# Performance work log

Measured on AMD Instinct MI355X. Metric: run time of the kernel, lower is better.

## Reference

```python
import jax, jax.numpy as jnp
import numpy as np

B, L, C = 8, 1024, 1024
H, DK = 16, 64
E, HID = 16, 64
CAP_FACTOR = 0.5
EPS = 1e-5


def setup_inputs() -> dict:
    key = jax.random.key(0)
    ks = jax.random.split(key, 20)
    f32 = jnp.float32
    s_c = 1.0 / np.sqrt(C)
    s_h = 1.0 / np.sqrt(HID)
    inp = {
        "qx": jax.random.normal(ks[0], (B, L, C), f32),
        "kx": jax.random.normal(ks[1], (B, L, C), f32),
        "vx": jax.random.normal(ks[2], (B, L, C), f32),
        "maskPAD": jnp.ones((B, L), dtype=bool),
        # attention params (torch Linear weight layout [out,in])
        "WQ": jax.random.normal(ks[3], (H * DK, C), f32) * s_c,
        "bQ": jnp.zeros((H * DK,), f32),
        "WK": jax.random.normal(ks[4], (H * DK, C), f32) * s_c,
        "bK": jnp.zeros((H * DK,), f32),
        "WV": jax.random.normal(ks[5], (H * DK, C), f32) * s_c,
        "bV": jnp.zeros((H * DK,), f32),
        "WO": jax.random.normal(ks[6], (C, H * DK), f32) * s_c,
        "bO": jnp.zeros((C,), f32),
        "ln1_w": jnp.ones((C,), f32),
        "ln1_b": jnp.zeros((C,), f32),
        # router
        "Wsw": jax.random.normal(ks[7], (E, C), f32) * s_c,
        "bsw": jnp.zeros((E,), f32),
        # per-expert FFN: Linear(C,HID) -> ReLU -> Linear(HID,C)
        "W1": jax.random.normal(ks[8], (E, C, HID), f32) * s_c,
        "b1": jnp.zeros((E, HID), f32),
        "W2": jax.random.normal(ks[9], (E, HID, C), f32) * s_h,
        "b2": jnp.zeros((E, C), f32),
    }
    return inp


def _layernorm(x, w, b):
    mu = jnp.mean(x, axis=-1, keepdims=True)
    var = jnp.mean(jnp.square(x - mu), axis=-1, keepdims=True)
    return (x - mu) * jax.lax.rsqrt(var + EPS) * w + b


def _moe(x2d, Wsw, bsw, W1, b1, W2, b2):
    # x2d: [N, C] tokens; top-1 switch routing with capacity-based token dropping
    N = x2d.shape[0]
    cap = int(CAP_FACTOR * N / E)
    logits = x2d @ Wsw.T + bsw                      # [N, E]
    probs = jax.nn.softmax(logits, axis=-1)
    routes = jnp.argmax(probs, axis=-1)             # [N]
    pmax = jnp.max(probs, axis=-1)                  # [N]
    onehot = jax.nn.one_hot(routes, E, dtype=jnp.int32)
    # position of each token within its expert's queue (deterministic order;
    # torch uses randperm before dropping -- math identical up to permutation)
    pos = jnp.take_along_axis(jnp.cumsum(onehot, axis=0) - 1, routes[:, None], axis=1)[:, 0]
    kept = pos < cap
    slot = jnp.where(kept, routes * cap + pos, E * cap)  # dropped -> trash slot
    buf = jnp.zeros((E * cap + 1, x2d.shape[1]), x2d.dtype).at[slot].set(x2d)
    eb = buf[: E * cap].reshape(E, cap, -1)         # [E, cap, C]
    h = jax.nn.relu(jnp.einsum("ecd,edh->ech", eb, W1) + b1[:, None, :])
    y = jnp.einsum("ech,ehd->ecd", h, W2) + b2[:, None, :]
    yflat = y.reshape(E * cap, -1)
    gathered = yflat[jnp.where(kept, routes * cap + pos, 0)]
    final = jnp.where(kept[:, None], gathered, x2d)  # dropped tokens pass through
    # is_scale_prob=False: multiply by p/stop_grad(p) (==1 in fwd, grads flow)
    scale = pmax / jax.lax.stop_gradient(pmax)
    return final * scale[:, None]


def reference(qx, kx, vx, maskPAD, WQ, bQ, WK, bK, WV, bV, WO, bO,
              ln1_w, ln1_b, Wsw, bsw, W1, b1, W2, b2):
    # multi-head attention (maskPAD is unused in the original SelfAttention_1)
    q = (qx @ WQ.T + bQ).reshape(B, L, H, DK)
    k = (kx @ WK.T + bK).reshape(B, L, H, DK)
    v = (vx @ WV.T + bV).reshape(B, L, H, DK)
    scores = jnp.einsum("bqhd,bkhd->bhqk", q, k) / np.sqrt(DK).astype(np.float32)
    alpha = jax.nn.softmax(scores, axis=-1)
    z = jnp.einsum("bhqk,bkhd->bqhd", alpha, v).reshape(B, L, H * DK)
    att = z @ WO.T + bO
    zn = _layernorm(qx + att, ln1_w, ln1_b)          # norm1 residual
    moe_out = _moe(zn.reshape(B * L, C), Wsw, bsw, W1, b1, W2, b2).reshape(B, L, C)
    out = zn + moe_out                               # note: norm2 unused in original
    return (out, kx, vx, maskPAD)
```

## Files before the change

### kernel.cpp

```cpp
#include <hip/hip_runtime.h>


typedef __bf16 bf16;
typedef __bf16 bf16x4 __attribute__((ext_vector_type(4)));
typedef __bf16 bf16x8 __attribute__((ext_vector_type(8)));
typedef float  f32x4  __attribute__((ext_vector_type(4)));

#define NB    8
#define LL    1024
#define CC    1024
#define NH    16
#define DKD   64
#define NE    16
#define NHID  64
#define CAP   256
#define NTOK  (NB*LL)
#define MB    (1024*1024)

__device__ __forceinline__ void gload16(const bf16* g, bf16* l)
{
    __builtin_amdgcn_global_load_lds(
        (const __attribute__((address_space(1))) void*)g,
        (__attribute__((address_space(3))) void*)l, 16, 0, 0);
}

__device__ inline void split3v(const f32x4 v, bf16x4& a, bf16x4& b, bf16x4& c)
{
#pragma unroll
    for (int k = 0; k < 4; k++) {
        const float x  = v[k];
        const bf16  hi = (bf16)x;
        const float r1 = x - (float)hi;
        const bf16  md = (bf16)r1;
        const float r2 = r1 - (float)md;
        a[k] = hi; b[k] = md; c[k] = (bf16)r2;
    }
}

__device__ inline bf16x8 pack8(const bf16x4 a, const bf16x4 b)
{
    bf16x8 r;
#pragma unroll
    for (int e = 0; e < 4; e++) { r[e] = a[e]; r[4 + e] = b[e]; }
    return r;
}

__global__ __launch_bounds__(256)
void split3(const float* __restrict__ z, bf16* __restrict__ z1,
            bf16* __restrict__ z2, bf16* __restrict__ z3)
{
    const size_t i = ((size_t)blockIdx.x * 256 + threadIdx.x) * 4;
    const f32x4 v = *(const f32x4*)(z + i);
    bf16x4 a, b, c;
    split3v(v, a, b, c);
    *(bf16x4*)(z1 + i) = a;
    *(bf16x4*)(z2 + i) = b;
    *(bf16x4*)(z3 + i) = c;
}

__global__ __launch_bounds__(512)
void gemm_limb6(const bf16* __restrict__ A0, const bf16* __restrict__ A1,
                const bf16* __restrict__ A2,
                const bf16* __restrict__ W0, const bf16* __restrict__ W1l,
                const bf16* __restrict__ W2l,
                const float* __restrict__ bias, float* __restrict__ C,
                int M, int N, int K)
{
    __shared__ __align__(16) bf16 As[2][3][128][32];
    __shared__ __align__(16) bf16 Ws[2][3][128][32];

    const int tid  = threadIdx.x;
    const int lane = tid & 63;
    const int wv   = tid >> 6;
    const int bm = blockIdx.x * 128;
    const int bn = blockIdx.y * 128;
    const int wm = (wv & 1) * 64;
    const int wn = (wv >> 1) * 32;
    const int lr = lane & 15;
    const int lq = lane >> 4;

    const int r0  = tid >> 2;
    const int cc8 = (tid & 3) * 8;

    const bf16* Aps[3] = {A0, A1, A2};
    const bf16* Wps[3] = {W0, W1l, W2l};

    f32x4 acc[4][2];
#pragma unroll
    for (int i = 0; i < 4; i++)
#pragma unroll
        for (int j = 0; j < 2; j++) acc[i][j] = f32x4{0.f, 0.f, 0.f, 0.f};

    constexpr int PI[6] = {0, 0, 1, 1, 0, 2};
    constexpr int PJ[6] = {0, 1, 0, 1, 2, 0};

#pragma unroll
    for (int l = 0; l < 3; l++) {
        gload16(Aps[l] + (size_t)(bm + r0) * K + cc8, &As[0][l][r0][cc8]);
        gload16(Wps[l] + (size_t)(bn + r0) * K + cc8, &Ws[0][l][r0][cc8]);
    }
    __syncthreads();

    int cur = 0;
    const int NT = K / 32;
    for (int t = 0; t < NT; t++) {
        if (t < NT - 1) {
            const int k1 = (t + 1) * 32;
#pragma unroll
            for (int l = 0; l < 3; l++) {
                gload16(Aps[l] + (size_t)(bm + r0) * K + k1 + cc8,
                        &As[cur ^ 1][l][r0][cc8]);
                gload16(Wps[l] + (size_t)(bn + r0) * K + k1 + cc8,
                        &Ws[cur ^ 1][l][r0][cc8]);
            }
        }

        bf16x8 af[3][4], bfr[3][2];
#pragma unroll
        for (int i = 0; i < 4; i++) {
            af[0][i] = *(const bf16x8*)&As[cur][0][wm + i * 16 + lr][lq * 8];
            af[1][i] = *(const bf16x8*)&As[cur][1][wm + i * 16 + lr][lq * 8];
            af[2][i] = *(const bf16x8*)&As[cur][2][wm + i * 16 + lr][lq * 8];
        }
#pragma unroll
        for (int j = 0; j < 2; j++) {
            bfr[0][j] = *(const bf16x8*)&Ws[cur][0][wn + j * 16 + lr][lq * 8];
            bfr[1][j] = *(const bf16x8*)&Ws[cur][1][wn + j * 16 + lr][lq * 8];
            bfr[2][j] = *(const bf16x8*)&Ws[cur][2][wn + j * 16 + lr][lq * 8];
        }
#pragma unroll
        for (int p = 0; p < 6; p++)
#pragma unroll
            for (int i = 0; i < 4; i++)
#pragma unroll
                for (int j = 0; j < 2; j++)
                    acc[i][j] = __builtin_amdgcn_mfma_f32_16x16x32_bf16(
                        af[PI[p]][i], bfr[PJ[p]][j], acc[i][j], 0, 0, 0);

        __syncthreads();
        cur ^= 1;
    }

#pragma unroll
    for (int i = 0; i < 4; i++)
#pragma unroll
        for (int j = 0; j < 2; j++) {
            const int col = bn + wn + j * 16 + lr;
            const float bv = bias[col];
#pragma unroll
            for (int r = 0; r < 4; r++) {
                const int row = bm + wm + i * 16 + lq * 4 + r;
                C[(size_t)row * N + col] = acc[i][j][r] + bv;
            }
        }
}

__global__ __launch_bounds__(256)
void vsplit(const float* __restrict__ Vf, bf16* __restrict__ T0,
            bf16* __restrict__ T1, bf16* __restrict__ T2)
{
    __shared__ __align__(16) bf16 Lt[3][64][72];
    const int tid = threadIdx.x;
    const int bh  = blockIdx.x;
    const int b   = bh >> 4, h = bh & 15;
    const int l0  = blockIdx.y * 64;

    const int dql = tid & 15;
    const int lrr = tid >> 4;
#pragma unroll
    for (int p = 0; p < 4; p++) {
        const int l = p * 16 + lrr;
        const f32x4 v = *(const f32x4*)(
            Vf + (size_t)(b * LL + l0 + l) * 1024 + h * 64 + dql * 4);
        bf16x4 a, bq, c; split3v(v, a, bq, c);
#pragma unroll
        for (int e = 0; e < 4; e++) {
            Lt[0][dql * 4 + e][l] = a[e];
            Lt[1][dql * 4 + e][l] = bq[e];
            Lt[2][dql * 4 + e][l] = c[e];
        }
    }
    __syncthreads();
    const int d  = tid >> 2;
    const int lc = tid & 3;
    const size_t o = (size_t)bh * 65536 + (size_t)d * 1024 + l0 + lc * 16;
    *(bf16x8*)(T0 + o)     = *(const bf16x8*)&Lt[0][d][lc * 16];
    *(bf16x8*)(T0 + o + 8) = *(const bf16x8*)&Lt[0][d][lc * 16 + 8];
    *(bf16x8*)(T1 + o)     = *(const bf16x8*)&Lt[1][d][lc * 16];
    *(bf16x8*)(T1 + o + 8) = *(const bf16x8*)&Lt[1][d][lc * 16 + 8];
    *(bf16x8*)(T2 + o)     = *(const bf16x8*)&Lt[2][d][lc * 16];
    *(bf16x8*)(T2 + o + 8) = *(const bf16x8*)&Lt[2][d][lc * 16 + 8];
}

__global__ __launch_bounds__(256)
void flash_mfma(float* __restrict__ Qf, const float* __restrict__ Kf,
                const bf16* __restrict__ Vt0, const bf16* __restrict__ Vt1,
                const bf16* __restrict__ Vt2)
{
    __shared__ __align__(16) bf16  Ks[3][32][64];
    __shared__ __align__(16) bf16  Vs[3][64][32];
    __shared__ __align__(16) float Ps[128][32];

    const int tid  = threadIdx.x;
    const int lane = tid & 63;
    const int w    = tid >> 6;
    const int lr   = lane & 15;
    const int lq   = lane >> 4;
    const int lr7  = lr & 7;

    const int bid = (int)blockIdx.x;
    const int qb  = (bid >> 3) & 7;
    const int bh  = (bid & 7) * 16 + (bid >> 6);
    const int b   = bh >> 4, h = bh & 15;
    const int q0  = qb * 128;
    const size_t base = (size_t)b * LL * 1024 + (size_t)h * 64;

    bf16x8 qf[3][2][2];
#pragma unroll
    for (int mi = 0; mi < 2; mi++)
#pragma unroll
        for (int ks = 0; ks < 2; ks++) {
            const float* src = Qf + base +
                (size_t)(q0 + w * 32 + mi * 16 + lr) * 1024 + ks * 32 + lq * 8;
            f32x4 v0 = *(const f32x4*)src;
            f32x4 v1 = *(const f32x4*)(src + 4);
            v0 *= 0.125f; v1 *= 0.125f;
            bf16x4 a0, b0, c0, a1, b1, c1;
            split3v(v0, a0, b0, c0);
            split3v(v1, a1, b1, c1);
            qf[0][mi][ks] = pack8(a0, a1);
            qf[1][mi][ks] = pack8(b0, b1);
            qf[2][mi][ks] = pack8(c0, c1);
        }

    const int kr  = tid >> 3, kq = tid & 7;
    const int kpg = kq ^ (kr & 7);
    const int vr  = tid >> 2, vg = tid & 3;
    const int vlg = vg ^ ((vr >> 1) & 3);
    const float* kbase = Kf + base + (size_t)kr * 1024 + kq * 8;
    const size_t vtb = (size_t)bh * 65536 + (size_t)vr * 1024 + (size_t)vlg * 8;

    f32x4  kp0 = *(const f32x4*)(kbase);
    f32x4  kp1 = *(const f32x4*)(kbase + 4);
    bf16x8 vp0 = *(const bf16x8*)(Vt0 + vtb);
    bf16x8 vp1 = *(const bf16x8*)(Vt1 + vtb);
    bf16x8 vp2 = *(const bf16x8*)(Vt2 + vtb);

    float m_[2][4], l_[2][4];
    f32x4 accO[2][4];
#pragma unroll
    for (int mi = 0; mi < 2; mi++)
#pragma unroll
        for (int rr = 0; rr < 4; rr++) { m_[mi][rr] = -3.0e38f; l_[mi][rr] = 0.f; }
#pragma unroll
    for (int mi = 0; mi < 2; mi++)
#pragma unroll
        for (int nd = 0; nd < 4; nd++) accO[mi][nd] = f32x4{0.f, 0.f, 0.f, 0.f};

    constexpr int PI[6] = {0, 0, 1, 1, 0, 2};
    constexpr int PJ[6] = {0, 1, 0, 1, 2, 0};

    for (int kt = 0; kt < 32; kt++) {
        __syncthreads();
        {
            bf16x4 a0, b0, c0, a1, b1, c1;
            split3v(kp0, a0, b0, c0);
            split3v(kp1, a1, b1, c1);
            *(bf16x8*)&Ks[0][kr][kpg * 8] = pack8(a0, a1);
            *(bf16x8*)&Ks[1][kr][kpg * 8] = pack8(b0, b1);
            *(bf16x8*)&Ks[2][kr][kpg * 8] = pack8(c0, c1);
            *(bf16x8*)&Vs[0][vr][vg * 8] = vp0;
            *(bf16x8*)&Vs[1][vr][vg * 8] = vp1;
            *(bf16x8*)&Vs[2][vr][vg * 8] = vp2;
        }
        __syncthreads();
        if (kt < 31) {
            const float* ks_ = kbase + (size_t)(kt + 1) * 32 * 1024;
            kp0 = *(const f32x4*)ks_;
            kp1 = *(const f32x4*)(ks_ + 4);
            const size_t vo = vtb + (size_t)(kt + 1) * 32;
            vp0 = *(const bf16x8*)(Vt0 + vo);
            vp1 = *(const bf16x8*)(Vt1 + vo);
            vp2 = *(const bf16x8*)(Vt2 + vo);
        }

        f32x4 accS[2][2];
#pragma unroll
        for (int mi = 0; mi < 2; mi++)
#pragma unroll
            for (int nj = 0; nj < 2; nj++) accS[mi][nj] = f32x4{0.f, 0.f, 0.f, 0.f};
#pragma unroll
        for (int nj = 0; nj < 2; nj++) {
            bf16x8 kfr[3][2];
#pragma unroll
            for (int ks = 0; ks < 2; ks++) {
                const int kg = (ks * 4 + lq) ^ lr7;
                kfr[0][ks] = *(const bf16x8*)&Ks[0][nj * 16 + lr][kg * 8];
                kfr[1][ks] = *(const bf16x8*)&Ks[1][nj * 16 + lr][kg * 8];
                kfr[2][ks] = *(const bf16x8*)&Ks[2][nj * 16 + lr][kg * 8];
            }
#pragma unroll
            for (int p = 0; p < 6; p++)
#pragma unroll
                for (int mi = 0; mi < 2; mi++)
#pragma unroll
                    for (int ks = 0; ks < 2; ks++)
                        accS[mi][nj] = __builtin_amdgcn_mfma_f32_16x16x32_bf16(
                            qf[PI[p]][mi][ks], kfr[PJ[p]][ks], accS[mi][nj], 0, 0, 0);
        }

#pragma unroll
        for (int mi = 0; mi < 2; mi++)
#pragma unroll
            for (int rr = 0; rr < 4; rr++) {
                const float s0 = accS[mi][0][rr], s1 = accS[mi][1][rr];
                float t = fmaxf(s0, s1);
                t = fmaxf(t, __shfl_xor(t, 1));
                t = fmaxf(t, __shfl_xor(t, 2));
                t = fmaxf(t, __shfl_xor(t, 4));
                t = fmaxf(t, __shfl_xor(t, 8));
                const float mnew  = fmaxf(m_[mi][rr], t);
                const float alpha = expf(m_[mi][rr] - mnew);
                const float p0 = expf(s0 - mnew);
                const float p1 = expf(s1 - mnew);
                float ps = p0 + p1;
                ps += __shfl_xor(ps, 1);
                ps += __shfl_xor(ps, 2);
                ps += __shfl_xor(ps, 4);
                ps += __shfl_xor(ps, 8);
                l_[mi][rr] = l_[mi][rr] * alpha + ps;
                m_[mi][rr] = mnew;
                const int prow = w * 32 + mi * 16 + lq * 4 + rr;
                const int pr7  = prow & 7;
                Ps[prow][(((lr >> 2) ^ pr7) << 2) | (lr & 3)]       = p0;
                Ps[prow][(((4 + (lr >> 2)) ^ pr7) << 2) | (lr & 3)] = p1;
#pragma unroll
                for (int nd = 0; nd < 4; nd++) accO[mi][nd][rr] *= alpha;
            }

        bf16x8 pf[3][2];
#pragma unroll
        for (int mi = 0; mi < 2; mi++) {
            const int row = w * 32 + mi * 16 + lr;
            const f32x4 v0 = *(const f32x4*)&Ps[row][((2 * lq) ^ lr7) * 4];
            const f32x4 v1 = *(const f32x4*)&Ps[row][((2 * lq + 1) ^ lr7) * 4];
            bf16x4 a0, b0, c0, a1, b1, c1;
            split3v(v0, a0, b0, c0);
            split3v(v1, a1, b1, c1);
            pf[0][mi] = pack8(a0, a1);
            pf[1][mi] = pack8(b0, b1);
            pf[2][mi] = pack8(c0, c1);
        }

        const int vgp = lq ^ ((lr >> 1) & 3);
#pragma unroll
        for (int nd = 0; nd < 4; nd++) {
            bf16x8 vfr[3];
            vfr[0] = *(const bf16x8*)&Vs[0][nd * 16 + lr][vgp * 8];
            vfr[1] = *(const bf16x8*)&Vs[1][nd * 16 + lr][vgp * 8];
            vfr[2] = *(const bf16x8*)&Vs[2][nd * 16 + lr][vgp * 8];
#pragma unroll
            for (int p = 0; p < 6; p++)
#pragma unroll
                for (int mi = 0; mi < 2; mi++)
                    accO[mi][nd] = __builtin_amdgcn_mfma_f32_16x16x32_bf16(
                        pf[PI[p]][mi], vfr[PJ[p]], accO[mi][nd], 0, 0, 0);
        }
    }

#pragma unroll
    for (int mi = 0; mi < 2; mi++) {
        float inv[4];
#pragma unroll
        for (int rr = 0; rr < 4; rr++) inv[rr] = 1.f / l_[mi][rr];
#pragma unroll
        for (int nd = 0; nd < 4; nd++)
#pragma unroll
            for (int rr = 0; rr < 4; rr++)
                Qf[base + (size_t)(q0 + w * 32 + mi * 16 + lq * 4 + rr) * 1024 +
                   nd * 16 + lr] = accO[mi][nd][rr] * inv[rr];
    }
}

__global__ __launch_bounds__(256)
void ln_kernel(const float* __restrict__ qx, const float* __restrict__ att,
               const float* __restrict__ w, const float* __restrict__ bch,
               float* __restrict__ zn)
{
    const int row = blockIdx.x, tid = threadIdx.x;
    const size_t off = (size_t)row * 1024 + tid * 4;
    const f32x4 q4 = *(const f32x4*)(qx + off);
    const f32x4 a4 = *(const f32x4*)(att + off);
    float x[4];
#pragma unroll
    for (int i = 0; i < 4; i++) x[i] = q4[i] + a4[i];

    __shared__ float red[8];
    float part = x[0] + x[1] + x[2] + x[3];
#pragma unroll
    for (int d = 1; d < 64; d <<= 1) part += __shfl_xor(part, d);
    if ((tid & 63) == 0) red[tid >> 6] = part;
    __syncthreads();
    const float mu = (red[0] + red[1] + red[2] + red[3]) * (1.f / 1024.f);

    float p2 = 0.f;
#pragma unroll
    for (int i = 0; i < 4; i++) { const float d = x[i] - mu; p2 += d * d; }
#pragma unroll
    for (int d = 1; d < 64; d <<= 1) p2 += __shfl_xor(p2, d);
    if ((tid & 63) == 0) red[4 + (tid >> 6)] = p2;
    __syncthreads();
    const float var  = (red[4] + red[5] + red[6] + red[7]) * (1.f / 1024.f);
    const float rstd = 1.f / sqrtf(var + 1e-5f);

    const f32x4 w4 = *(const f32x4*)(w + tid * 4);
    const f32x4 b4 = *(const f32x4*)(bch + tid * 4);
    f32x4 out;
#pragma unroll
    for (int i = 0; i < 4; i++)
        out[i] = (x[i] - mu) * rstd * w4[i] + b4[i];
    *(f32x4*)(zn + off) = out;
}

__global__ __launch_bounds__(64)
void router_kernel(const float* __restrict__ zn, const float* __restrict__ Wsw,
                   const float* __restrict__ bsw, int* __restrict__ routes)
{
    const int t = blockIdx.x, lane = threadIdx.x;
    const float* x = zn + (size_t)t * 1024;
    float acc[16];
#pragma unroll
    for (int e = 0; e < 16; e++) acc[e] = 0.f;
    for (int ii = 0; ii < 16; ii++) {
        const float xv = x[lane + 64 * ii];
#pragma unroll
        for (int e = 0; e < 16; e++)
            acc[e] += xv * Wsw[e * 1024 + lane + 64 * ii];
    }
#pragma unroll
    for (int e = 0; e < 16; e++)
#pragma unroll
        for (int d = 1; d < 64; d <<= 1) acc[e] += __shfl_xor(acc[e], d);
    if (lane == 0) {
        float best = acc[0] + bsw[0];
        int bi = 0;
#pragma unroll
        for (int e = 1; e < 16; e++) {
            const float lg = acc[e] + bsw[e];
            if (lg > best) { best = lg; bi = e; }
        }
        routes[t] = bi;
    }
}

__global__ __launch_bounds__(1024)
void route_scan(const int* __restrict__ routes, int* __restrict__ slot_of_token,
                int* __restrict__ token_of_slot)
{
    const int wv = threadIdx.x >> 6;
    const int lane = threadIdx.x & 63;
    int cnt = 0;
    for (int c = 0; c < NTOK / 64; c++) {
        const int tok = c * 64 + lane;
        const bool match = (routes[tok] == wv);
        const unsigned long long mask = __ballot(match);
        const int pos = cnt + __popcll(mask & ((1ull << lane) - 1ull));
        if (match) {
            if (pos < CAP) {
                slot_of_token[tok] = wv * CAP + pos;
                token_of_slot[wv * CAP + pos] = tok;
            } else slot_of_token[tok] = -1;
        }
        cnt += __popcll(mask);
    }
    const int filled = cnt < CAP ? cnt : CAP;
    for (int s2 = filled + lane; s2 < CAP; s2 += 64)
        token_of_slot[wv * CAP + s2] = -1;
}

__global__ __launch_bounds__(64)
void ffn1(const float* __restrict__ zn, const int* __restrict__ token_of_slot,
          const float* __restrict__ W1, const float* __restrict__ b1,
          float* __restrict__ hbuf)
{
    const int s = blockIdx.x, lane = threadIdx.x;
    const int tok = token_of_slot[s];
    if (tok < 0) return;
    const int e = s >> 8;
    const float* w = W1 + (size_t)e * CC * NHID + lane;
    const float* x = zn + (size_t)tok * 1024;
    float acc = 0.f;
#pragma unroll 8
    for (int i = 0; i < 1024; i++) acc += x[i] * w[(size_t)i * NHID];
    acc += b1[e * NHID + lane];
    hbuf[(size_t)s * NHID + lane] = fmaxf(acc, 0.f);
}

__global__ __launch_bounds__(256)
void ffn2(const float* __restrict__ hbuf, const int* __restrict__ token_of_slot,
          const float* __restrict__ W2, const float* __restrict__ b2,
          float* __restrict__ ybuf)
{
    const int s = blockIdx.x, tid = threadIdx.x;
    const int tok = token_of_slot[s];
    if (tok < 0) return;
    const int e = s >> 8;
    const int c0 = tid * 4;
    const float* w = W2 + (size_t)e * NHID * CC + c0;
    const float* hrow = hbuf + (size_t)s * NHID;
    const f32x4 b4 = *(const f32x4*)(b2 + e * CC + c0);
    float a0 = b4[0], a1 = b4[1], a2 = b4[2], a3 = b4[3];
#pragma unroll 8
    for (int k = 0; k < NHID; k++) {
        const float hv = hrow[k];
        const f32x4 w4 = *(const f32x4*)(w + (size_t)k * CC);
        a0 += hv * w4[0]; a1 += hv * w4[1];
        a2 += hv * w4[2]; a3 += hv * w4[3];
    }
    const f32x4 out = {a0, a1, a2, a3};
    *(f32x4*)(ybuf + (size_t)s * 1024 + c0) = out;
}

__global__ __launch_bounds__(256)
void assemble(const float* __restrict__ zn, const float* __restrict__ ybuf,
              const int* __restrict__ slot_of_token, float* __restrict__ out)
{
    const int tok = blockIdx.x, tid = threadIdx.x;
    const int slot = slot_of_token[tok];
    const size_t off = (size_t)tok * 1024 + tid * 4;
    const f32x4 z4 = *(const f32x4*)(zn + off);
    f32x4 m4;
    if (slot >= 0) m4 = *(const f32x4*)(ybuf + (size_t)slot * 1024 + tid * 4);
    else           m4 = z4;
    f32x4 o;
#pragma unroll
    for (int i = 0; i < 4; i++) o[i] = z4[i] + m4[i];
    *(f32x4*)(out + off) = o;
}

__global__ __launch_bounds__(256)
void fill_mask(float* __restrict__ p, int n)
{
    const int i = blockIdx.x * 256 + threadIdx.x;
    if (i < n) p[i] = 1.0f;
}

extern "C" void kernel_launch(void* const* d_in, const int* in_sizes, int n_in,
                              void* d_out, int out_size, void* d_ws, size_t ws_size,
                              hipStream_t stream)
{
    (void)out_size; (void)ws_size;
    const float* qx = (const float*)d_in[0];
    const float* kx = (const float*)d_in[1];
    const float* vx = (const float*)d_in[2];
    int wbase = 4;
    if (n_in >= 4 && in_sizes[3] != NB * LL) wbase = 3;
    const float* WQ   = (const float*)d_in[wbase + 0];
    const float* bQ   = (const float*)d_in[wbase + 1];
    const float* WK   = (const float*)d_in[wbase + 2];
    const float* bK   = (const float*)d_in[wbase + 3];
    const float* WV   = (const float*)d_in[wbase + 4];
    const float* bV   = (const float*)d_in[wbase + 5];
    const float* WO   = (const float*)d_in[wbase + 6];
    const float* bO   = (const float*)d_in[wbase + 7];
    const float* ln1w = (const float*)d_in[wbase + 8];
    const float* ln1b = (const float*)d_in[wbase + 9];
    const float* Wsw  = (const float*)d_in[wbase + 10];
    const float* bsw  = (const float*)d_in[wbase + 11];
    const float* W1   = (const float*)d_in[wbase + 12];
    const float* b1   = (const float*)d_in[wbase + 13];
    const float* W2   = (const float*)d_in[wbase + 14];
    const float* b2   = (const float*)d_in[wbase + 15];

    char* D   = (char*)d_out;
    char* wsb = (char*)d_ws;

    float* Qbuf = (float*)(wsb);
    bf16*  la0  = (bf16*)(D);
    bf16*  la1  = (bf16*)(D + (size_t)16 * MB);
    bf16*  la2  = (bf16*)(wsb + (size_t)32 * MB);
    bf16*  lw0  = (bf16*)(wsb + (size_t)48 * MB);
    bf16*  lw1  = (bf16*)(wsb + (size_t)50 * MB);
    bf16*  lw2  = (bf16*)(wsb + (size_t)52 * MB);
    float* Kbuf = (float*)(D + (size_t)32 * MB);
    float* Vbuf = (float*)(D + (size_t)64 * MB);

    const dim3 gblk(NTOK / 128, CC / 128, 1);
    const int GA = NTOK * 1024 / 1024;
    const int GW = CC * 1024 / 1024;

    split3<<<GA, 256, 0, stream>>>(qx, la0, la1, la2);
    split3<<<GW, 256, 0, stream>>>(WQ, lw0, lw1, lw2);
    gemm_limb6<<<gblk, 512, 0, stream>>>(la0, la1, la2, lw0, lw1, lw2, bQ, Qbuf, NTOK, CC, CC);
    split3<<<GA, 256, 0, stream>>>(kx, la0, la1, la2);
    split3<<<GW, 256, 0, stream>>>(WK, lw0, lw1, lw2);
    gemm_limb6<<<gblk, 512, 0, stream>>>(la0, la1, la2, lw0, lw1, lw2, bK, Kbuf, NTOK, CC, CC);
    split3<<<GA, 256, 0, stream>>>(vx, la0, la1, la2);
    split3<<<GW, 256, 0, stream>>>(WV, lw0, lw1, lw2);
    gemm_limb6<<<gblk, 512, 0, stream>>>(la0, la1, la2, lw0, lw1, lw2, bV, Vbuf, NTOK, CC, CC);

    bf16* Vt0 = la0;
    bf16* Vt1 = la1;
    bf16* Vt2 = la2;
    vsplit<<<dim3(128, 16), 256, 0, stream>>>(Vbuf, Vt0, Vt1, Vt2);

    flash_mfma<<<1024, 256, 0, stream>>>(Qbuf, Kbuf, Vt0, Vt1, Vt2);

    split3<<<GA, 256, 0, stream>>>(Qbuf, la0, la1, la2);
    split3<<<GW, 256, 0, stream>>>(WO, lw0, lw1, lw2);
    float* attbuf = Kbuf;
    gemm_limb6<<<gblk, 512, 0, stream>>>(la0, la1, la2, lw0, lw1, lw2, bO, attbuf, NTOK, CC, CC);

    float* znbuf = Vbuf;
    ln_kernel<<<NTOK, 256, 0, stream>>>(qx, attbuf, ln1w, ln1b, znbuf);

    int*   routes        = (int*)(wsb + (size_t)32 * MB);
    int*   slot_of_token = (int*)(wsb + (size_t)32 * MB + 64 * 1024);
    int*   token_of_slot = (int*)(wsb + (size_t)32 * MB + 128 * 1024);
    float* hbuf          = (float*)(wsb + (size_t)33 * MB);
    float* ybuf          = (float*)(wsb + (size_t)34 * MB);

    router_kernel<<<NTOK, 64, 0, stream>>>(znbuf, Wsw, bsw, routes);
    route_scan<<<1, 1024, 0, stream>>>(routes, slot_of_token, token_of_slot);
    ffn1<<<NE * CAP, 64, 0, stream>>>(znbuf, token_of_slot, W1, b1, hbuf);
    ffn2<<<NE * CAP, 256, 0, stream>>>(hbuf, token_of_slot, W2, b2, ybuf);

    assemble<<<NTOK, 256, 0, stream>>>(znbuf, ybuf, slot_of_token, (float*)d_out);

    hipMemcpyAsync(D + (size_t)32 * MB, (const void*)kx,
                   (size_t)NTOK * 1024 * 4, hipMemcpyDeviceToDevice, stream);
    hipMemcpyAsync(D + (size_t)64 * MB, (const void*)vx,
                   (size_t)NTOK * 1024 * 4, hipMemcpyDeviceToDevice, stream);
    fill_mask<<<NTOK / 256, 256, 0, stream>>>((float*)d_out + (size_t)3 * NTOK * 1024, NTOK);
}
```

Measured before the change: 1.200 ms.

## Triple-buffer LDS in limb GEMM with explicit vmcnt waits for deeper prefetch

Changes the 3-limb bf16 GEMM from double to triple buffering. Tiles are now prefetched two k-steps ahead, and the full __syncthreads is replaced by a partial s_waitcnt vmcnt plus s_barrier, so loads for the next stage can stay in flight across the barrier. This is meant to hide global-to-LDS latency better. In exchange, LDS use grows from 96KB to 144KB per block, which may lower occupancy, and correctness now depends on the manual vmcnt count of 6 matching the number of outstanding loads per stage.

```diff
diff --git a/kernel.cpp b/kernel.cpp
--- a/kernel.cpp
+++ b/kernel.cpp
@@ -66,8 +66,8 @@
                 const float* __restrict__ bias, float* __restrict__ C,
                 int M, int N, int K)
 {
-    __shared__ __align__(16) bf16 As[2][3][128][32];
-    __shared__ __align__(16) bf16 Ws[2][3][128][32];
+    __shared__ __align__(16) bf16 As[3][3][128][32];
+    __shared__ __align__(16) bf16 Ws[3][3][128][32];
 
     const int tid  = threadIdx.x;
     const int lane = tid & 63;
@@ -94,25 +94,29 @@
     constexpr int PI[6] = {0, 0, 1, 1, 0, 2};
     constexpr int PJ[6] = {0, 1, 0, 1, 2, 0};
 
-#pragma unroll
-    for (int l = 0; l < 3; l++) {
-        gload16(Aps[l] + (size_t)(bm + r0) * K + cc8, &As[0][l][r0][cc8]);
-        gload16(Wps[l] + (size_t)(bn + r0) * K + cc8, &Ws[0][l][r0][cc8]);
-    }
-    __syncthreads();
+#define STAGE(T, BUF)                                                          \
+    {                                                                          \
+        const int kk_ = (T) * 32;                                              \
+        _Pragma("unroll")                                                      \
+        for (int l = 0; l < 3; l++) {                                          \
+            gload16(Aps[l] + (size_t)(bm + r0) * K + kk_ + cc8,                \
+                    &As[BUF][l][r0][cc8]);                                     \
+            gload16(Wps[l] + (size_t)(bn + r0) * K + kk_ + cc8,                \
+                    &Ws[BUF][l][r0][cc8]);                                     \
+        }                                                                      \
+    }
+
+    const int NT = K / 32;
+    STAGE(0, 0);
+    STAGE(1, 1);
+    asm volatile("s_waitcnt vmcnt(6)" ::: "memory");
+    __builtin_amdgcn_s_barrier();
 
     int cur = 0;
-    const int NT = K / 32;
     for (int t = 0; t < NT; t++) {
-        if (t < NT - 1) {
-            const int k1 = (t + 1) * 32;
-#pragma unroll
-            for (int l = 0; l < 3; l++) {
-                gload16(Aps[l] + (size_t)(bm + r0) * K + k1 + cc8,
-                        &As[cur ^ 1][l][r0][cc8]);
-                gload16(Wps[l] + (size_t)(bn + r0) * K + k1 + cc8,
-                        &Ws[cur ^ 1][l][r0][cc8]);
-            }
+        if (t + 2 < NT) {
+            const int nb = (cur + 2 >= 3) ? cur - 1 : cur + 2;
+            STAGE(t + 2, nb);
         }
 
         bf16x8 af[3][4], bfr[3][2];
@@ -137,9 +141,15 @@
                     acc[i][j] = __builtin_amdgcn_mfma_f32_16x16x32_bf16(
                         af[PI[p]][i], bfr[PJ[p]][j], acc[i][j], 0, 0, 0);
 
-        __syncthreads();
-        cur ^= 1;
-    }
+        if (t + 2 < NT) {
+            asm volatile("s_waitcnt vmcnt(6)" ::: "memory");
+        } else if (t + 1 < NT) {
+            asm volatile("s_waitcnt vmcnt(0)" ::: "memory");
+        }
+        __builtin_amdgcn_s_barrier();
+        cur = (cur + 1 >= 3) ? 0 : cur + 1;
+    }
+#undef STAGE
 
 #pragma unroll
     for (int i = 0; i < 4; i++)
```

Result: no change. 1.215 ms (+1.2%).
